# Performance work log

Hardware: AMD Instinct MI355X
Metric: run time of the kernel (lower is better)

Reference implementation:

```python
import jax, jax.numpy as jnp
import numpy as np

T, I, H, O = 4096, 512, 1024, 256


def setup_inputs() -> dict:
    key = jax.random.key(0)
    ks = jax.random.split(key, 11)
    sx = np.sqrt(2.0 / (I + H)).astype(np.float32)
    sh = np.sqrt(1.0 / H).astype(np.float32)
    sy = np.sqrt(2.0 / (H + O)).astype(np.float32)
    inp = {
        "x": jax.random.normal(ks[0], (T, I), jnp.float32),
        "Wx_forget": jax.random.normal(ks[1], (H, I), jnp.float32) * sx,
        "Wh_forget": jax.random.normal(ks[2], (H, H), jnp.float32) * sh,
        "b_forget": jnp.zeros((H,), jnp.float32),
        "Wx_input": jax.random.normal(ks[3], (H, I), jnp.float32) * sx,
        "Wh_input": jax.random.normal(ks[4], (H, H), jnp.float32) * sh,
        "b_input": jnp.zeros((H,), jnp.float32),
        "Wx_candidate": jax.random.normal(ks[5], (H, I), jnp.float32) * sx,
        "Wh_candidate": jax.random.normal(ks[6], (H, H), jnp.float32) * sh,
        "b_candidate": jnp.zeros((H,), jnp.float32),
        "Wx_update": jax.random.normal(ks[7], (H, I), jnp.float32) * sx,
        "Wh_update": jax.random.normal(ks[8], (H, H), jnp.float32) * sh,
        "bh_update": jnp.zeros((H,), jnp.float32),
        "Wy": jax.random.normal(ks[9], (O, H), jnp.float32) * sy,
        "by": jnp.zeros((O,), jnp.float32),
    }
    return inp


def reference(x, Wx_forget, Wh_forget, b_forget, Wx_input, Wh_input, b_input,
              Wx_candidate, Wh_candidate, b_candidate, Wx_update, Wh_update,
              bh_update, Wy, by):
    H_ = Wh_forget.shape[0]
    # Precompute input projections for all timesteps as one GEMM per gate: [T, H]
    gx_f = x @ Wx_forget.T + b_forget
    gx_i = x @ Wx_input.T + b_input
    gx_c = x @ Wx_candidate.T + b_candidate
    gx_o = x @ Wx_update.T + bh_update

    def step(carry, gx_t):
        h, c = carry
        gf, gi, gc, go = gx_t
        f_t = jax.nn.sigmoid(gf + Wh_forget @ h)
        i_t = jax.nn.sigmoid(gi + Wh_input @ h)
        cand = jnp.tanh(gc + Wh_candidate @ h)
        c_t = f_t * c + i_t * cand
        o_t = jax.nn.sigmoid(go + Wh_update @ h)
        h_t = o_t * c_t  # NOTE: original omits tanh(c_t)
        return (h_t, c_t), h_t

    h0 = jnp.zeros((H_,), x.dtype)
    c0 = jnp.zeros((H_,), x.dtype)
    _, hs = jax.lax.scan(step, (h0, c0), (gx_f, gx_i, gx_c, gx_o))
    y = hs @ Wy.T + by  # [T, O]
    return y.reshape(-1)
```

## Files before the change

kernel.cpp:

```cpp
#include <hip/hip_runtime.h>
#include <hip/hip_fp16.h>

#define T_DIM 4096
#define I_DIM 512
#define H_DIM 1024
#define O_DIM 256

#define NWG 64
#define RTHREADS 256

typedef _Float16 half2v __attribute__((ext_vector_type(2)));
typedef unsigned int u32x4 __attribute__((ext_vector_type(4)));

__device__ __forceinline__ float sigmoid_fast(float x) {
    return 1.f / (1.f + __expf(-x));
}
__device__ __forceinline__ float tanh_fast(float x) {
    float ax = fabsf(x);
    float e  = __expf(-2.f * ax);
    float t  = (1.f - e) / (1.f + e);
    return copysignf(t, x);
}

__device__ __forceinline__ float dot2u(unsigned int a, unsigned int b, float c) {
#if __has_builtin(__builtin_amdgcn_fdot2)
    return __builtin_amdgcn_fdot2(__builtin_bit_cast(half2v, a),
                                  __builtin_bit_cast(half2v, b), c, false);
#else
    half2v ha = __builtin_bit_cast(half2v, a);
    half2v hb = __builtin_bit_cast(half2v, b);
    return c + (float)ha.x * (float)hb.x + (float)ha.y * (float)hb.y;
#endif
}

__device__ __forceinline__ u32x4 load_l3(const u32x4* p) {
    u32x4 r;
    asm volatile("global_load_dwordx4 %0, %1, off sc0 sc1\n\t"
                 "s_waitcnt vmcnt(0)"
                 : "=v"(r) : "v"(p) : "memory");
    return r;
}
__device__ __forceinline__ void store_l3(u32x4* p, u32x4 v) {
    asm volatile("global_store_dwordx4 %0, %1, off sc0 sc1"
                 :: "v"(p), "v"(v) : "memory");
}

__global__ void pack_wx_bias(const float* __restrict__ wxf, const float* __restrict__ wxi,
                             const float* __restrict__ wxc, const float* __restrict__ wxo,
                             const float* __restrict__ bf,  const float* __restrict__ bi,
                             const float* __restrict__ bc,  const float* __restrict__ bo,
                             float* __restrict__ wxp, float* __restrict__ bpack) {
    int idx = blockIdx.x * 256 + threadIdx.x;
    const int total = 4 * H_DIM * I_DIM;
    if (idx < total) {
        int R = idx >> 9;
        int k = idx & (I_DIM - 1);
        int g = R >> 10;
        int h = R & (H_DIM - 1);
        const float* w = (g == 0) ? wxf : (g == 1) ? wxi : (g == 2) ? wxc : wxo;
        wxp[idx] = w[h * I_DIM + k];
    }
    if (idx < 4 * H_DIM) {
        int g = idx >> 10, h = idx & (H_DIM - 1);
        const float* b = (g == 0) ? bf : (g == 1) ? bi : (g == 2) ? bc : bo;
        bpack[idx] = b[h];
    }
}

__global__ void pack_wh_f16(const float* __restrict__ whf, const float* __restrict__ whi,
                            const float* __restrict__ whc, const float* __restrict__ who,
                            __half* __restrict__ wh16) {
    int d = blockIdx.x * 256 + threadIdx.x;
    if (d >= 4 * H_DIM * H_DIM) return;
    int u4  = d >> 3;
    int h8  = d & 7;
    int wg  = u4 >> 13;
    int rem = u4 & 8191;
    int i   = rem >> 8;
    int tid = rem & 255;
    int e = i * 8 + h8;
    int g = (tid >> 6) & 3;
    int jj = (tid >> 2) & 15;
    int q = tid & 3;
    int j = wg * 16 + jj;
    int k = q * 256 + e;
    const float* w = (g == 0) ? whf : (g == 1) ? whi : (g == 2) ? whc : who;
    wh16[d] = __float2half(w[j * H_DIM + k]);
}

#define BM 64
#define BN 64
#define BK 16
__global__ __launch_bounds__(256) void gemm_bt(const float* __restrict__ A,
                                               const float* __restrict__ B,
                                               const float* __restrict__ bias,
                                               float* __restrict__ C,
                                               int M, int N, int K) {
    __shared__ float As[BK][BM + 4];
    __shared__ float Bs[BK][BN + 4];
    int tid = threadIdx.x;
    int m0 = blockIdx.y * BM, n0 = blockIdx.x * BN;
    int tx = tid & 15, ty = tid >> 4;
    float acc[4][4] = {};
    for (int k0 = 0; k0 < K; k0 += BK) {
#pragma unroll
        for (int l = 0; l < 4; ++l) {
            int idx = tid + l * 256;
            int m = idx >> 4, k = idx & 15;
            As[k][m] = A[(long)(m0 + m) * K + k0 + k];
            Bs[k][m] = B[(long)(n0 + m) * K + k0 + k];
        }
        __syncthreads();
#pragma unroll
        for (int kk = 0; kk < BK; ++kk) {
            float ra[4], rb[4];
#pragma unroll
            for (int i = 0; i < 4; ++i) ra[i] = As[kk][ty * 4 + i];
#pragma unroll
            for (int j = 0; j < 4; ++j) rb[j] = Bs[kk][tx * 4 + j];
#pragma unroll
            for (int i = 0; i < 4; ++i)
#pragma unroll
                for (int j = 0; j < 4; ++j) acc[i][j] += ra[i] * rb[j];
        }
        __syncthreads();
    }
#pragma unroll
    for (int i = 0; i < 4; ++i) {
        int m = m0 + ty * 4 + i;
#pragma unroll
        for (int j = 0; j < 4; ++j) {
            int n = n0 + tx * 4 + j;
            C[(long)m * N + n] = acc[i][j] + bias[n];
        }
    }
}

__global__ __launch_bounds__(RTHREADS, 1) void lstm_recurrence(
    const float* __restrict__ gx,
    const uint4* __restrict__ wh16,
    u32x4* __restrict__ bc,
    float* __restrict__ hs) {
    extern __shared__ uint4 wlds[];
    const int wg = blockIdx.x, tid = threadIdx.x;
    const int g = (tid >> 6) & 3;
    const int jj = (tid >> 2) & 15;
    const int q = tid & 3;
    const int j = wg * 16 + jj;
    const int R = g * H_DIM + j;

    __shared__ float lds_gate[4][16];
    __shared__ float lds_c[16];
    __shared__ unsigned short lds_pub[16];
    __shared__ unsigned int __attribute__((aligned(16))) lds_h32[512];
    if (tid < 16) lds_c[tid] = 0.f;

    const uint4* wsrc = wh16 + (long)wg * 8192;
#pragma unroll
    for (int i = 0; i < 32; ++i) wlds[i * 256 + tid] = wsrc[i * 256 + tid];

    const int pL = tid & 63, pc = tid >> 6;

    float gx_next = gx[R];
    __syncthreads();

    for (int t = 0; t < T_DIM; ++t) {
        float gxv = gx_next;
        if (t + 1 < T_DIM) gx_next = gx[(long)(t + 1) * (4 * H_DIM) + R];

        {
            const unsigned int target = (unsigned int)t;
            const u32x4* addr = bc + (size_t)(t & 1) * 512 + pL * 8 + pc;
            u32x4 v;
            do {
                v = load_l3(addr);
            } while (v.x != target || v.w != target);
            lds_h32[pL * 8 + pc * 2]     = v.y;
            lds_h32[pL * 8 + pc * 2 + 1] = v.z;
        }
        __syncthreads();

        const uint4* hlds = (const uint4*)lds_h32 + q * 32;
        float a0 = 0.f, a1 = 0.f, a2 = 0.f, a3 = 0.f;
#pragma unroll
        for (int i = 0; i < 32; ++i) {
            uint4 hv = hlds[i];
            uint4 wv = wlds[i * 256 + tid];
            a0 = dot2u(hv.x, wv.x, a0);
            a1 = dot2u(hv.y, wv.y, a1);
            a2 = dot2u(hv.z, wv.z, a2);
            a3 = dot2u(hv.w, wv.w, a3);
        }
        float s = (a0 + a1) + (a2 + a3);
        s += __shfl_xor(s, 1);
        s += __shfl_xor(s, 2);
        if (q == 0) lds_gate[g][jj] = s + gxv;
        __syncthreads();

        float hn = 0.f;
        if (tid < 16) {
            float gf = lds_gate[0][tid], gi = lds_gate[1][tid];
            float gc = lds_gate[2][tid], go = lds_gate[3][tid];
            float c  = lds_c[tid];
            float f  = sigmoid_fast(gf);
            float ii = sigmoid_fast(gi);
            float cd = tanh_fast(gc);
            float o  = sigmoid_fast(go);
            float cn = f * c + ii * cd;
            hn = o * cn;
            lds_c[tid] = cn;
            lds_pub[tid] = __half_as_ushort(__float2half(hn));
        }
        if (tid < 4) {
            unsigned int stamp = (unsigned int)(t + 1);
            unsigned int u0 = (unsigned int)lds_pub[4 * tid] |
                              ((unsigned int)lds_pub[4 * tid + 1] << 16);
            unsigned int u1 = (unsigned int)lds_pub[4 * tid + 2] |
                              ((unsigned int)lds_pub[4 * tid + 3] << 16);
            u32x4 out; out.x = stamp; out.y = u0; out.z = u1; out.w = stamp;
            store_l3(bc + (size_t)((t + 1) & 1) * 512 + wg * 8 + tid, out);
        }
        if (tid < 16) {
            hs[(long)t * H_DIM + wg * 16 + tid] = hn;
        }
    }
}

extern "C" void kernel_launch(void* const* d_in, const int* in_sizes, int n_in,
                              void* d_out, int out_size, void* d_ws, size_t ws_size,
                              hipStream_t stream) {
    (void)in_sizes; (void)n_in; (void)out_size; (void)ws_size;
    const float* x    = (const float*)d_in[0];
    const float* wxf  = (const float*)d_in[1];
    const float* whf  = (const float*)d_in[2];
    const float* bf   = (const float*)d_in[3];
    const float* wxi  = (const float*)d_in[4];
    const float* whi  = (const float*)d_in[5];
    const float* bi   = (const float*)d_in[6];
    const float* wxc  = (const float*)d_in[7];
    const float* whc  = (const float*)d_in[8];
    const float* bc_  = (const float*)d_in[9];
    const float* wxo  = (const float*)d_in[10];
    const float* who  = (const float*)d_in[11];
    const float* bo   = (const float*)d_in[12];
    const float* wy   = (const float*)d_in[13];
    const float* by   = (const float*)d_in[14];
    float* y_out = (float*)d_out;

    char* base = (char*)d_ws;
    float*  gx    = (float*)(base + 0);
    float*  wxp   = (float*)(base + (size_t)64 * 1024 * 1024);
    float*  bpack = (float*)(base + (size_t)72 * 1024 * 1024);
    __half* wh16  = (__half*)(base + (size_t)72 * 1024 * 1024 + 16384);
    float*  hs    = (float*)(base + (size_t)80 * 1024 * 1024 + 16384);
    u32x4*  bcast = (u32x4*)(base + (size_t)96 * 1024 * 1024 + 16384);

    hipFuncSetAttribute((const void*)lstm_recurrence,
                        hipFuncAttributeMaxDynamicSharedMemorySize, 128 * 1024);

    hipMemsetAsync(bcast, 0, 16384, stream);

    pack_wx_bias<<<(4 * H_DIM * I_DIM + 255) / 256, 256, 0, stream>>>(
        wxf, wxi, wxc, wxo, bf, bi, bc_, bo, wxp, bpack);
    pack_wh_f16<<<(4 * H_DIM * H_DIM + 255) / 256, 256, 0, stream>>>(
        whf, whi, whc, who, wh16);

    gemm_bt<<<dim3((4 * H_DIM) / BN, T_DIM / BM), 256, 0, stream>>>(
        x, wxp, bpack, gx, T_DIM, 4 * H_DIM, I_DIM);

    lstm_recurrence<<<NWG, RTHREADS, 128 * 1024, stream>>>(
        gx, (const uint4*)wh16, bcast, hs);

    gemm_bt<<<dim3(O_DIM / BN, T_DIM / BM), 256, 0, stream>>>(
        hs, wy, by, y_out, T_DIM, O_DIM, H_DIM);
}
```

Measured before the change: 10.71 ms.

## Spread LSTM recurrence across 256 workgroups with 4 hidden units each

Splits the persistent recurrence kernel across 256 workgroups instead of 64, so each owns 4 hidden units and keeps a 32KB fp16 slice of the recurrent weights in static LDS. Each thread now does a shorter dot product (8 iterations) followed by a 16-lane shuffle reduction, and the h-vector staging buffer is padded to avoid bank conflicts. The Wh packing layout and the broadcast buffer indexing are changed to match. The aim is to cut the per-step matvec latency on the critical path. In exchange, every step's grid-wide spin-wait now spans four times as many workgroups.

```diff
diff --git a/kernel.cpp b/kernel.cpp
--- a/kernel.cpp
+++ b/kernel.cpp
@@ -6,7 +6,7 @@
 #define H_DIM 1024
 #define O_DIM 256
 
-#define NWG 64
+#define NWG 256
 #define RTHREADS 256
 
 typedef _Float16 half2v __attribute__((ext_vector_type(2)));
@@ -74,18 +74,18 @@
     if (d >= 4 * H_DIM * H_DIM) return;
     int u4  = d >> 3;
     int h8  = d & 7;
-    int wg  = u4 >> 13;
-    int rem = u4 & 8191;
+    int w   = u4 >> 11;
+    int rem = u4 & 2047;
     int i   = rem >> 8;
     int tid = rem & 255;
-    int e = i * 8 + h8;
-    int g = (tid >> 6) & 3;
-    int jj = (tid >> 2) & 15;
-    int q = tid & 3;
-    int j = wg * 16 + jj;
-    int k = q * 256 + e;
-    const float* w = (g == 0) ? whf : (g == 1) ? whi : (g == 2) ? whc : who;
-    wh16[d] = __float2half(w[j * H_DIM + k]);
+    int e  = i * 8 + h8;
+    int g  = tid >> 6;
+    int jj = (tid >> 4) & 3;
+    int s  = tid & 15;
+    int j  = w * 4 + jj;
+    int k  = s * 64 + e;
+    const float* wsrc = (g == 0) ? whf : (g == 1) ? whi : (g == 2) ? whc : who;
+    wh16[d] = __float2half(wsrc[j * H_DIM + k]);
 }
 
 #define BM 64
@@ -138,67 +138,68 @@
 
 __global__ __launch_bounds__(RTHREADS, 1) void lstm_recurrence(
     const float* __restrict__ gx,
-    const uint4* __restrict__ wh16,
+    const uint4* __restrict__ wpk,
     u32x4* __restrict__ bc,
     float* __restrict__ hs) {
-    extern __shared__ uint4 wlds[];
-    const int wg = blockIdx.x, tid = threadIdx.x;
-    const int g = (tid >> 6) & 3;
-    const int jj = (tid >> 2) & 15;
-    const int q = tid & 3;
-    const int j = wg * 16 + jj;
-    const int R = g * H_DIM + j;
-
-    __shared__ float lds_gate[4][16];
-    __shared__ float lds_c[16];
-    __shared__ unsigned short lds_pub[16];
-    __shared__ unsigned int __attribute__((aligned(16))) lds_h32[512];
-    if (tid < 16) lds_c[tid] = 0.f;
-
-    const uint4* wsrc = wh16 + (long)wg * 8192;
-#pragma unroll
-    for (int i = 0; i < 32; ++i) wlds[i * 256 + tid] = wsrc[i * 256 + tid];
-
-    const int pL = tid & 63, pc = tid >> 6;
-
-    float gx_next = gx[R];
+    __shared__ uint4 wlds[2048];
+    __shared__ unsigned int __attribute__((aligned(16))) hldsp[16 * 36];
+    __shared__ float lds_gate[4][4];
+    __shared__ float lds_c[4];
+    __shared__ unsigned short lds_pub[4];
+
+    const int w = blockIdx.x, tid = threadIdx.x;
+    const int g  = tid >> 6;
+    const int jj = (tid >> 4) & 3;
+    const int s  = tid & 15;
+    const int R  = g * H_DIM + w * 4 + jj;
+
+    if (tid < 4) lds_c[tid] = 0.f;
+
+    const uint4* wsrc = wpk + (long)w * 2048;
+#pragma unroll
+    for (int i = 0; i < 8; ++i) wlds[i * 256 + tid] = wsrc[i * 256 + tid];
+
+    float gx_next = (s == 0) ? gx[R] : 0.f;
     __syncthreads();
 
     for (int t = 0; t < T_DIM; ++t) {
         float gxv = gx_next;
-        if (t + 1 < T_DIM) gx_next = gx[(long)(t + 1) * (4 * H_DIM) + R];
+        if (s == 0 && t + 1 < T_DIM)
+            gx_next = gx[(long)(t + 1) * (4 * H_DIM) + R];
 
         {
             const unsigned int target = (unsigned int)t;
-            const u32x4* addr = bc + (size_t)(t & 1) * 512 + pL * 8 + pc;
+            const u32x4* addr = bc + (size_t)(t & 1) * NWG + tid;
             u32x4 v;
             do {
                 v = load_l3(addr);
             } while (v.x != target || v.w != target);
-            lds_h32[pL * 8 + pc * 2]     = v.y;
-            lds_h32[pL * 8 + pc * 2 + 1] = v.z;
-        }
-        __syncthreads();
-
-        const uint4* hlds = (const uint4*)lds_h32 + q * 32;
+            int ss = tid >> 4, oo = (tid * 2) & 31;
+            hldsp[ss * 36 + oo]     = v.y;
+            hldsp[ss * 36 + oo + 1] = v.z;
+        }
+        __syncthreads();
+
         float a0 = 0.f, a1 = 0.f, a2 = 0.f, a3 = 0.f;
 #pragma unroll
-        for (int i = 0; i < 32; ++i) {
-            uint4 hv = hlds[i];
+        for (int i = 0; i < 8; ++i) {
+            uint4 hv = ((const uint4*)hldsp)[s * 9 + i];
             uint4 wv = wlds[i * 256 + tid];
             a0 = dot2u(hv.x, wv.x, a0);
             a1 = dot2u(hv.y, wv.y, a1);
             a2 = dot2u(hv.z, wv.z, a2);
             a3 = dot2u(hv.w, wv.w, a3);
         }
-        float s = (a0 + a1) + (a2 + a3);
-        s += __shfl_xor(s, 1);
-        s += __shfl_xor(s, 2);
-        if (q == 0) lds_gate[g][jj] = s + gxv;
+        float sum = (a0 + a1) + (a2 + a3);
+        sum += __shfl_xor(sum, 1);
+        sum += __shfl_xor(sum, 2);
+        sum += __shfl_xor(sum, 4);
+        sum += __shfl_xor(sum, 8);
+        if (s == 0) lds_gate[g][jj] = sum + gxv;
         __syncthreads();
 
         float hn = 0.f;
-        if (tid < 16) {
+        if (tid < 4) {
             float gf = lds_gate[0][tid], gi = lds_gate[1][tid];
             float gc = lds_gate[2][tid], go = lds_gate[3][tid];
             float c  = lds_c[tid];
@@ -211,17 +212,15 @@
             lds_c[tid] = cn;
             lds_pub[tid] = __half_as_ushort(__float2half(hn));
         }
+        if (tid == 0) {
+            unsigned int stamp = (unsigned int)(t + 1);
+            unsigned int u0 = (unsigned int)lds_pub[0] | ((unsigned int)lds_pub[1] << 16);
+            unsigned int u1 = (unsigned int)lds_pub[2] | ((unsigned int)lds_pub[3] << 16);
+            u32x4 out; out.x = stamp; out.y = u0; out.z = u1; out.w = stamp;
+            store_l3(bc + (size_t)((t + 1) & 1) * NWG + w, out);
+        }
         if (tid < 4) {
-            unsigned int stamp = (unsigned int)(t + 1);
-            unsigned int u0 = (unsigned int)lds_pub[4 * tid] |
-                              ((unsigned int)lds_pub[4 * tid + 1] << 16);
-            unsigned int u1 = (unsigned int)lds_pub[4 * tid + 2] |
-                              ((unsigned int)lds_pub[4 * tid + 3] << 16);
-            u32x4 out; out.x = stamp; out.y = u0; out.z = u1; out.w = stamp;
-            store_l3(bc + (size_t)((t + 1) & 1) * 512 + wg * 8 + tid, out);
-        }
-        if (tid < 16) {
-            hs[(long)t * H_DIM + wg * 16 + tid] = hn;
+            hs[(long)t * H_DIM + w * 4 + tid] = hn;
         }
     }
 }
@@ -255,9 +254,6 @@
     float*  hs    = (float*)(base + (size_t)80 * 1024 * 1024 + 16384);
     u32x4*  bcast = (u32x4*)(base + (size_t)96 * 1024 * 1024 + 16384);
 
-    hipFuncSetAttribute((const void*)lstm_recurrence,
-                        hipFuncAttributeMaxDynamicSharedMemorySize, 128 * 1024);
-
     hipMemsetAsync(bcast, 0, 16384, stream);
 
     pack_wx_bias<<<(4 * H_DIM * I_DIM + 255) / 256, 256, 0, stream>>>(
@@ -268,7 +264,7 @@
     gemm_bt<<<dim3((4 * H_DIM) / BN, T_DIM / BM), 256, 0, stream>>>(
         x, wxp, bpack, gx, T_DIM, 4 * H_DIM, I_DIM);
 
-    lstm_recurrence<<<NWG, RTHREADS, 128 * 1024, stream>>>(
+    lstm_recurrence<<<NWG, RTHREADS, 0, stream>>>(
         gx, (const uint4*)wh16, bcast, hs);
 
     gemm_bt<<<dim3(O_DIM / BN, T_DIM / BM), 256, 0, stream>>>(
```

Measured after the change: 9.801 ms. -8.5%, faster.
